# Performance work log

Hardware: AMD Instinct MI355X
Metric: run time of the kernel (lower is better)

## Reference

```python
import jax, jax.numpy as jnp
import numpy as np

B, S, H = 4, 2048, 1024

def setup_inputs() -> dict:
    key = jax.random.key(0)
    k = jax.random.split(key, 5)
    scale = 1.0 / np.sqrt(H)
    return {
        "hidden": jax.random.normal(k[0], (B, S, H), dtype=jnp.float32),
        "mask": jnp.zeros((B, 1, S, S), dtype=jnp.float32),
        "R": jax.random.normal(k[1], (S, S), dtype=jnp.float32),
        "G_w": jax.random.normal(k[2], (H, H), dtype=jnp.float32) * scale,
        "G_b": jnp.zeros((H,), dtype=jnp.float32),
        "F_w": jax.random.normal(k[3], (H, H), dtype=jnp.float32) * scale,
        "F_b": jnp.zeros((H,), dtype=jnp.float32),
    }

def reference(hidden, mask, R, G_w, G_b, F_w, F_b):
    # scores: [B, S, S] = learned random bias + additive attention mask
    scores = R + mask[:, 0]
    probs = jax.nn.softmax(scores, axis=-1)  # dropout is identity in eval mode
    values = jnp.einsum('bsh,oh->bso', hidden, G_w) + G_b  # G_linear
    out = jnp.einsum('bqk,bkh->bqh', probs, values)
    out = jnp.einsum('bsh,oh->bso', out, F_w) + F_b  # final_linear
    return out
```

## Files before the change

### kernel.cpp

```cpp
#include <hip/hip_runtime.h>
#include <hip/hip_bf16.h>

typedef __bf16 bf16x8 __attribute__((ext_vector_type(8)));
typedef __bf16 bf16x4 __attribute__((ext_vector_type(4)));
typedef float  f32x16 __attribute__((ext_vector_type(16)));

#define GPTR(p) ((__attribute__((address_space(1))) void*)(p))
#define LPTR(p) ((__attribute__((address_space(3))) void*)(p))

__global__ __launch_bounds__(256) void pre_kernel(
    const float* __restrict__ Fw, __bf16* __restrict__ f_bf,
    const float* __restrict__ Gw, __bf16* __restrict__ gt_bf,
    const float* __restrict__ Gb, const float* __restrict__ Fb,
    float* __restrict__ b2,
    const float* __restrict__ hidden, __bf16* __restrict__ xh, int H) {
    __shared__ float tile[64][65];
    const int blk = blockIdx.x;
    const int t = threadIdx.x;

    if (blk < 512) {
        long i = ((long)blk * 256 + t) * 8;
        float4 a = *reinterpret_cast<const float4*>(Fw + i);
        float4 c = *reinterpret_cast<const float4*>(Fw + i + 4);
        bf16x8 o;
        o[0] = (__bf16)a.x; o[1] = (__bf16)a.y; o[2] = (__bf16)a.z; o[3] = (__bf16)a.w;
        o[4] = (__bf16)c.x; o[5] = (__bf16)c.y; o[6] = (__bf16)c.z; o[7] = (__bf16)c.w;
        *reinterpret_cast<bf16x8*>(f_bf + i) = o;
    } else if (blk < 768) {
        const int id = blk - 512;
        const int bx = (id & 15) * 64;
        const int by = (id >> 4) * 64;
        const int tr = t >> 4;
        const int tc = (t & 15) * 4;
#pragma unroll
        for (int i = 0; i < 4; i++) {
            float4 v = *reinterpret_cast<const float4*>(&Gw[(size_t)(by + tr + i * 16) * H + bx + tc]);
            tile[tr + i * 16][tc + 0] = v.x;
            tile[tr + i * 16][tc + 1] = v.y;
            tile[tr + i * 16][tc + 2] = v.z;
            tile[tr + i * 16][tc + 3] = v.w;
        }
        __syncthreads();
        const int wr = t >> 2;
        const int wc = (t & 3) * 16;
        bf16x8 o0, o1;
#pragma unroll
        for (int j = 0; j < 8; j++) o0[j] = (__bf16)tile[wc + j][wr];
#pragma unroll
        for (int j = 0; j < 8; j++) o1[j] = (__bf16)tile[wc + 8 + j][wr];
        *reinterpret_cast<bf16x8*>(&gt_bf[(size_t)(bx + wr) * H + by + wc]) = o0;
        *reinterpret_cast<bf16x8*>(&gt_bf[(size_t)(bx + wr) * H + by + wc + 8]) = o1;
    } else if (blk < 1792) {
        const int o = blk - 768;
        float s = 0.f;
        for (int h = t; h < H; h += 256) s += Fw[(size_t)o * H + h] * Gb[h];
#pragma unroll
        for (int off = 32; off > 0; off >>= 1) s += __shfl_xor(s, off);
        __shared__ float ss[4];
        if ((t & 63) == 0) ss[t >> 6] = s;
        __syncthreads();
        if (t == 0) b2[o] = ss[0] + ss[1] + ss[2] + ss[3] + Fb[o];
    } else {
        const int id = blk - 1792;
        const long base = (long)id * 4096 + (long)t * 16;
        float4 v0 = *reinterpret_cast<const float4*>(hidden + base);
        float4 v1 = *reinterpret_cast<const float4*>(hidden + base + 4);
        float4 v2 = *reinterpret_cast<const float4*>(hidden + base + 8);
        float4 v3 = *reinterpret_cast<const float4*>(hidden + base + 12);
        bf16x8 o0, o1;
        o0[0] = (__bf16)v0.x; o0[1] = (__bf16)v0.y; o0[2] = (__bf16)v0.z; o0[3] = (__bf16)v0.w;
        o0[4] = (__bf16)v1.x; o0[5] = (__bf16)v1.y; o0[6] = (__bf16)v1.z; o0[7] = (__bf16)v1.w;
        o1[0] = (__bf16)v2.x; o1[1] = (__bf16)v2.y; o1[2] = (__bf16)v2.z; o1[3] = (__bf16)v2.w;
        o1[4] = (__bf16)v3.x; o1[5] = (__bf16)v3.y; o1[6] = (__bf16)v3.z; o1[7] = (__bf16)v3.w;
        *reinterpret_cast<bf16x8*>(xh + base) = o0;
        *reinterpret_cast<bf16x8*>(xh + base + 8) = o1;
    }
}

union MidSmem {
    struct { __bf16 a[64 * 64]; __bf16 b[64 * 64]; } g;
    float red[8];
};

__global__ __launch_bounds__(256) void mid_kernel(
    const __bf16* __restrict__ f_bf, const __bf16* __restrict__ gt_bf,
    __bf16* __restrict__ Wm,
    const float* __restrict__ R, const float* __restrict__ mask,
    __bf16* __restrict__ P, int H, int S) {
    __shared__ __align__(16) MidSmem sm;
    const int blk = blockIdx.x;
    const int t = threadIdx.x;

    if (blk < 256) {
        __bf16* As = sm.g.a;
        __bf16* Bs = sm.g.b;
        const int lane = t & 63;
        const int wave = t >> 6;
        const int lane31 = lane & 31;
        const int hi = lane >> 5;
        const int wm = (wave >> 1) * 32;
        const int wn = (wave & 1) * 32;
        const int bm = (blk >> 4) * 64;
        const int bn = (blk & 15) * 64;

        const int rsub = lane >> 3;
        const int csub = lane & 7;
        const int lchunk = csub ^ rsub;
        const __bf16* ga0 = f_bf + (size_t)(bm + wave * 16 + rsub) * H + lchunk * 8;
        const __bf16* gb0 = gt_bf + (size_t)(bn + wave * 16 + rsub) * H + lchunk * 8;

        f32x16 acc = (f32x16)(0.f);
        for (int kt = 0; kt < H; kt += 64) {
            __syncthreads();
#pragma unroll
            for (int c = 0; c < 2; c++)
                __builtin_amdgcn_global_load_lds(GPTR(ga0 + (size_t)(c * 8) * H + kt),
                                                 LPTR(&As[(wave * 16 + c * 8) * 64]), 16, 0, 0);
#pragma unroll
            for (int c = 0; c < 2; c++)
                __builtin_amdgcn_global_load_lds(GPTR(gb0 + (size_t)(c * 8) * H + kt),
                                                 LPTR(&Bs[(wave * 16 + c * 8) * 64]), 16, 0, 0);
            __syncthreads();
#pragma unroll
            for (int s = 0; s < 4; s++) {
                const int ra = wm + lane31;
                const int rb = wn + lane31;
                bf16x8 af = *reinterpret_cast<const bf16x8*>(
                    &As[ra * 64 + (((2 * s + hi) ^ (ra & 7)) << 3)]);
                bf16x8 bfr = *reinterpret_cast<const bf16x8*>(
                    &Bs[rb * 64 + (((2 * s + hi) ^ (rb & 7)) << 3)]);
                acc = __builtin_amdgcn_mfma_f32_32x32x16_bf16(af, bfr, acc, 0, 0, 0);
            }
        }
        const int cm = bm + wm;
        const int cn = bn + wn + lane31;
#pragma unroll
        for (int rq = 0; rq < 4; rq++) {
            const int rbase = rq * 8 + 4 * hi;
#pragma unroll
            for (int rr = 0; rr < 4; rr++)
                Wm[(size_t)(cm + rbase + rr) * H + cn] = (__bf16)acc[rq * 4 + rr];
        }
    } else {
        const int q = blk - 256;
        const int lane = t & 63, wave = t >> 6;
        const float* rrow = R + (size_t)q * S;

        float r[8];
#pragma unroll
        for (int i = 0; i < 2; i++) {
            float4 r4 = *reinterpret_cast<const float4*>(rrow + t * 8 + i * 4);
            r[i * 4 + 0] = r4.x; r[i * 4 + 1] = r4.y;
            r[i * 4 + 2] = r4.z; r[i * 4 + 3] = r4.w;
        }

        for (int b = 0; b < 4; b++) {
            const float* mrow = mask + ((size_t)b * S + q) * (size_t)S;
            __bf16* prow = P + ((size_t)b * S + q) * (size_t)S;

            float v[8];
#pragma unroll
            for (int i = 0; i < 2; i++) {
                float4 m4 = *reinterpret_cast<const float4*>(mrow + t * 8 + i * 4);
                v[i * 4 + 0] = r[i * 4 + 0] + m4.x;
                v[i * 4 + 1] = r[i * 4 + 1] + m4.y;
                v[i * 4 + 2] = r[i * 4 + 2] + m4.z;
                v[i * 4 + 3] = r[i * 4 + 3] + m4.w;
            }
            float mx = v[0];
#pragma unroll
            for (int i = 1; i < 8; i++) mx = fmaxf(mx, v[i]);
#pragma unroll
            for (int off = 32; off > 0; off >>= 1) mx = fmaxf(mx, __shfl_xor(mx, off));
            if (lane == 0) sm.red[wave] = mx;
            __syncthreads();
            mx = fmaxf(fmaxf(sm.red[0], sm.red[1]), fmaxf(sm.red[2], sm.red[3]));
            float sum = 0.f;
#pragma unroll
            for (int i = 0; i < 8; i++) { v[i] = __expf(v[i] - mx); sum += v[i]; }
#pragma unroll
            for (int off = 32; off > 0; off >>= 1) sum += __shfl_xor(sum, off);
            if (lane == 0) sm.red[4 + wave] = sum;
            __syncthreads();
            sum = sm.red[4] + sm.red[5] + sm.red[6] + sm.red[7];
            const float inv = 1.0f / sum;
            bf16x8 o;
#pragma unroll
            for (int i = 0; i < 8; i++) o[i] = (__bf16)(v[i] * inv);
            *reinterpret_cast<bf16x8*>(prow + t * 8) = o;
            __syncthreads();
        }
    }
}

__global__ __launch_bounds__(256) void gemm_wy_kernel(
    const __bf16* __restrict__ Wm, const __bf16* __restrict__ xh,
    __bf16* __restrict__ Yt) {
    constexpr int H = 1024, S = 2048, K = 1024;
    const int t = threadIdx.x;
    const int lane = t & 63;
    const int wave = t >> 6;
    const int lane31 = lane & 31;
    const int hi = lane >> 5;
    const int wm = (wave >> 1) * 64;
    const int wn = (wave & 1) * 64;
    const int id = blockIdx.x;
    const int xcd = id & 7;
    const int slot = id >> 3;
    const int bm = (slot & 7) * 128;
    const int bn = (xcd * 8 + (slot >> 3)) * 128;

    __shared__ __align__(16) __bf16 smem[32768];

    const int rsub = lane >> 3;
    const int csub = lane & 7;
    const int lchunk = csub ^ rsub;
    const __bf16* ga0 = Wm + (size_t)(bm + wave * 32 + rsub) * K + lchunk * 8;
    const __bf16* gb0 = xh + (size_t)(bn + wave * 32 + rsub) * K + lchunk * 8;

    auto stage = [&](int p, int kt) {
        __bf16* As_ = smem + p * 16384;
        __bf16* Bs_ = smem + p * 16384 + 8192;
#pragma unroll
        for (int c = 0; c < 4; c++)
            __builtin_amdgcn_global_load_lds(GPTR(ga0 + (size_t)(c * 8) * K + kt),
                                             LPTR(&As_[(wave * 32 + c * 8) * 64]), 16, 0, 0);
#pragma unroll
        for (int c = 0; c < 4; c++)
            __builtin_amdgcn_global_load_lds(GPTR(gb0 + (size_t)(c * 8) * K + kt),
                                             LPTR(&Bs_[(wave * 32 + c * 8) * 64]), 16, 0, 0);
    };

    f32x16 acc[2][2];
#pragma unroll
    for (int i = 0; i < 2; i++)
#pragma unroll
        for (int j = 0; j < 2; j++) acc[i][j] = (f32x16)(0.f);

    stage(0, 0);
    __syncthreads();
    int p = 0;
    for (int kt = 0; kt < K; kt += 64) {
        if (kt + 64 < K) stage(p ^ 1, kt + 64);
        const __bf16* As = smem + p * 16384;
        const __bf16* Bs = smem + p * 16384 + 8192;
#pragma unroll
        for (int s = 0; s < 4; s++) {
            bf16x8 af[2], bfr[2];
#pragma unroll
            for (int mi = 0; mi < 2; mi++) {
                const int r = wm + mi * 32 + lane31;
                af[mi] = *reinterpret_cast<const bf16x8*>(
                    &As[r * 64 + (((2 * s + hi) ^ (r & 7)) << 3)]);
            }
#pragma unroll
            for (int ni = 0; ni < 2; ni++) {
                const int r = wn + ni * 32 + lane31;
                bfr[ni] = *reinterpret_cast<const bf16x8*>(
                    &Bs[r * 64 + (((2 * s + hi) ^ (r & 7)) << 3)]);
            }
#pragma unroll
            for (int mi = 0; mi < 2; mi++)
#pragma unroll
                for (int ni = 0; ni < 2; ni++)
                    acc[mi][ni] = __builtin_amdgcn_mfma_f32_32x32x16_bf16(af[mi], bfr[ni], acc[mi][ni], 0, 0, 0);
        }
        __syncthreads();
        p ^= 1;
    }

#pragma unroll
    for (int mi = 0; mi < 2; mi++)
#pragma unroll
        for (int ni = 0; ni < 2; ni++) {
            const int cm = bm + wm + mi * 32;
            const int cnf = bn + wn + ni * 32 + lane31;
            __bf16* Cb = Yt + (size_t)(cnf >> 11) * H * S + (cnf & 2047);
#pragma unroll
            for (int rq = 0; rq < 4; rq++) {
                const int rbase = rq * 8 + 4 * hi;
#pragma unroll
                for (int rrq = 0; rrq < 4; rrq++)
                    Cb[(size_t)(cm + rbase + rrq) * S] = (__bf16)acc[mi][ni][rq * 4 + rrq];
            }
        }
}

template <bool CFLOAT, bool BIAS>
__global__ __launch_bounds__(256) void gemm_nt_kernel(
    const __bf16* __restrict__ A, const __bf16* __restrict__ B,
    const float* __restrict__ bias, void* __restrict__ Cv,
    int K, int lda, int ldb, int ldc,
    long strideA, long strideB, long strideC) {
    const int t = threadIdx.x;
    const int lane = t & 63;
    const int wave = t >> 6;
    const int lane31 = lane & 31;
    const int hi = lane >> 5;
    const int wm = (wave >> 1) * 64;
    const int wn = (wave & 1) * 64;
    const int id = blockIdx.x;
    const int xcd = id & 7;
    const int slot = id >> 3;
    const int bz = xcd >> 1;
    const int bm = ((xcd & 1) * 8 + (slot >> 3)) * 128;
    const int bn = (slot & 7) * 128;

    A += (size_t)bz * strideA;
    B += (size_t)bz * strideB;

    __shared__ __align__(16) __bf16 smem[32768];

    const int rsub = lane >> 3;
    const int csub = lane & 7;
    const int lchunk = csub ^ rsub;
    const __bf16* ga0 = A + (size_t)(bm + wave * 32 + rsub) * lda + lchunk * 8;
    const __bf16* gb0 = B + (size_t)(bn + wave * 32 + rsub) * ldb + lchunk * 8;

    auto stage = [&](int p, int kt) {
        __bf16* As_ = smem + p * 16384;
        __bf16* Bs_ = smem + p * 16384 + 8192;
#pragma unroll
        for (int c = 0; c < 4; c++)
            __builtin_amdgcn_global_load_lds(GPTR(ga0 + (size_t)(c * 8) * lda + kt),
                                             LPTR(&As_[(wave * 32 + c * 8) * 64]), 16, 0, 0);
#pragma unroll
        for (int c = 0; c < 4; c++)
            __builtin_amdgcn_global_load_lds(GPTR(gb0 + (size_t)(c * 8) * ldb + kt),
                                             LPTR(&Bs_[(wave * 32 + c * 8) * 64]), 16, 0, 0);
    };

    f32x16 acc[2][2];
#pragma unroll
    for (int i = 0; i < 2; i++)
#pragma unroll
        for (int j = 0; j < 2; j++) acc[i][j] = (f32x16)(0.f);

    stage(0, 0);
    __syncthreads();
    int p = 0;
    for (int kt = 0; kt < K; kt += 64) {
        if (kt + 64 < K) stage(p ^ 1, kt + 64);
        const __bf16* As = smem + p * 16384;
        const __bf16* Bs = smem + p * 16384 + 8192;
#pragma unroll
        for (int s = 0; s < 4; s++) {
            bf16x8 af[2], bfr[2];
#pragma unroll
            for (int mi = 0; mi < 2; mi++) {
                const int r = wm + mi * 32 + lane31;
                af[mi] = *reinterpret_cast<const bf16x8*>(
                    &As[r * 64 + (((2 * s + hi) ^ (r & 7)) << 3)]);
            }
#pragma unroll
            for (int ni = 0; ni < 2; ni++) {
                const int r = wn + ni * 32 + lane31;
                bfr[ni] = *reinterpret_cast<const bf16x8*>(
                    &Bs[r * 64 + (((2 * s + hi) ^ (r & 7)) << 3)]);
            }
#pragma unroll
            for (int mi = 0; mi < 2; mi++)
#pragma unroll
                for (int ni = 0; ni < 2; ni++)
                    acc[mi][ni] = __builtin_amdgcn_mfma_f32_32x32x16_bf16(af[mi], bfr[ni], acc[mi][ni], 0, 0, 0);
        }
        __syncthreads();
        p ^= 1;
    }

    __bf16* Cb = (__bf16*)Cv + (size_t)bz * strideC;
    float* Cf = (float*)Cv + (size_t)bz * strideC;
#pragma unroll
    for (int mi = 0; mi < 2; mi++)
#pragma unroll
        for (int ni = 0; ni < 2; ni++) {
            const int cm = bm + wm + mi * 32;
            const int cn = bn + wn + ni * 32 + lane31;
            const float bv = BIAS ? bias[cn] : 0.0f;
#pragma unroll
            for (int rq = 0; rq < 4; rq++) {
                const int rbase = rq * 8 + 4 * hi;
                if constexpr (CFLOAT) {
#pragma unroll
                    for (int rr = 0; rr < 4; rr++)
                        Cf[(size_t)(cm + rbase + rr) * ldc + cn] = acc[mi][ni][rq * 4 + rr] + bv;
                } else {
#pragma unroll
                    for (int rr = 0; rr < 4; rr++)
                        Cb[(size_t)(cm + rbase + rr) * ldc + cn] = (__bf16)(acc[mi][ni][rq * 4 + rr] + bv);
                }
            }
        }
}

extern "C" void kernel_launch(void* const* d_in, const int* in_sizes, int n_in,
                              void* d_out, int out_size, void* d_ws, size_t ws_size,
                              hipStream_t stream) {
    const float* hidden = (const float*)d_in[0];
    const float* mask   = (const float*)d_in[1];
    const float* R      = (const float*)d_in[2];
    const float* G_w    = (const float*)d_in[3];
    const float* G_b    = (const float*)d_in[4];
    const float* F_w    = (const float*)d_in[5];
    const float* F_b    = (const float*)d_in[6];
    float* out = (float*)d_out;

    constexpr int B = 4, S = 2048, H = 1024;
    char* ws = (char*)d_ws;
    __bf16* probs = (__bf16*)(ws);
    __bf16* yt    = (__bf16*)(ws + (32ll << 20));
    __bf16* xh    = (__bf16*)(ws + (48ll << 20));
    __bf16* f_bf  = (__bf16*)(ws + (64ll << 20));
    __bf16* gt_bf = (__bf16*)(ws + (66ll << 20));
    __bf16* Wm    = (__bf16*)(ws + (68ll << 20));
    float*  b2    = (float*)(ws + (70ll << 20));

    pre_kernel<<<3840, 256, 0, stream>>>(F_w, f_bf, G_w, gt_bf, G_b, F_b, b2,
                                         hidden, xh, H);

    mid_kernel<<<2304, 256, 0, stream>>>(f_bf, gt_bf, Wm, R, mask, probs, H, S);

    gemm_wy_kernel<<<512, 256, 0, stream>>>(Wm, xh, yt);

    gemm_nt_kernel<true, true><<<512, 256, 0, stream>>>(
        probs, yt, b2, out, S, S, S, H,
        (long)S * S, (long)H * S, (long)S * H);
}
```

Before: 228.4 us.

## Merge pre and mid kernels, convert weights to bf16 inside the W GEMM

Result: slower. 237.3 us (+3.9%).

```diff
diff --git a/kernel.cpp b/kernel.cpp
--- a/kernel.cpp
+++ b/kernel.cpp
@@ -8,60 +8,146 @@
 #define GPTR(p) ((__attribute__((address_space(1))) void*)(p))
 #define LPTR(p) ((__attribute__((address_space(3))) void*)(p))
 
-__global__ __launch_bounds__(256) void pre_kernel(
-    const float* __restrict__ Fw, __bf16* __restrict__ f_bf,
-    const float* __restrict__ Gw, __bf16* __restrict__ gt_bf,
+union MidSmem {
+    struct { __bf16 a[4096]; __bf16 b[4096]; float tile[32][65]; } g;
+    float red[8];
+};
+
+__global__ __launch_bounds__(256) void mid2_kernel(
+    const float* __restrict__ Fw, const float* __restrict__ Gw,
     const float* __restrict__ Gb, const float* __restrict__ Fb,
-    float* __restrict__ b2,
-    const float* __restrict__ hidden, __bf16* __restrict__ xh, int H) {
-    __shared__ float tile[64][65];
+    __bf16* __restrict__ Wm, float* __restrict__ b2,
+    const float* __restrict__ R, const float* __restrict__ mask,
+    __bf16* __restrict__ P,
+    const float* __restrict__ hidden, __bf16* __restrict__ xh,
+    int H, int S) {
+    __shared__ __align__(16) MidSmem sm;
     const int blk = blockIdx.x;
     const int t = threadIdx.x;
 
-    if (blk < 512) {
-        long i = ((long)blk * 256 + t) * 8;
-        float4 a = *reinterpret_cast<const float4*>(Fw + i);
-        float4 c = *reinterpret_cast<const float4*>(Fw + i + 4);
-        bf16x8 o;
-        o[0] = (__bf16)a.x; o[1] = (__bf16)a.y; o[2] = (__bf16)a.z; o[3] = (__bf16)a.w;
-        o[4] = (__bf16)c.x; o[5] = (__bf16)c.y; o[6] = (__bf16)c.z; o[7] = (__bf16)c.w;
-        *reinterpret_cast<bf16x8*>(f_bf + i) = o;
-    } else if (blk < 768) {
-        const int id = blk - 512;
-        const int bx = (id & 15) * 64;
-        const int by = (id >> 4) * 64;
-        const int tr = t >> 4;
-        const int tc = (t & 15) * 4;
-#pragma unroll
-        for (int i = 0; i < 4; i++) {
-            float4 v = *reinterpret_cast<const float4*>(&Gw[(size_t)(by + tr + i * 16) * H + bx + tc]);
-            tile[tr + i * 16][tc + 0] = v.x;
-            tile[tr + i * 16][tc + 1] = v.y;
-            tile[tr + i * 16][tc + 2] = v.z;
-            tile[tr + i * 16][tc + 3] = v.w;
-        }
-        __syncthreads();
-        const int wr = t >> 2;
-        const int wc = (t & 3) * 16;
-        bf16x8 o0, o1;
-#pragma unroll
-        for (int j = 0; j < 8; j++) o0[j] = (__bf16)tile[wc + j][wr];
-#pragma unroll
-        for (int j = 0; j < 8; j++) o1[j] = (__bf16)tile[wc + 8 + j][wr];
-        *reinterpret_cast<bf16x8*>(&gt_bf[(size_t)(bx + wr) * H + by + wc]) = o0;
-        *reinterpret_cast<bf16x8*>(&gt_bf[(size_t)(bx + wr) * H + by + wc + 8]) = o1;
-    } else if (blk < 1792) {
-        const int o = blk - 768;
-        float s = 0.f;
-        for (int h = t; h < H; h += 256) s += Fw[(size_t)o * H + h] * Gb[h];
-#pragma unroll
-        for (int off = 32; off > 0; off >>= 1) s += __shfl_xor(s, off);
-        __shared__ float ss[4];
-        if ((t & 63) == 0) ss[t >> 6] = s;
-        __syncthreads();
-        if (t == 0) b2[o] = ss[0] + ss[1] + ss[2] + ss[3] + Fb[o];
-    } else {
-        const int id = blk - 1792;
+    if (blk < 256) {
+        __bf16* As = sm.g.a;
+        __bf16* Bs = sm.g.b;
+        const int lane = t & 63;
+        const int wave = t >> 6;
+        const int lane31 = lane & 31;
+        const int hi = lane >> 5;
+        const int wm = (wave >> 1) * 32;
+        const int wn = (wave & 1) * 32;
+        const int bm = (blk >> 4) * 64;
+        const int bn = (blk & 15) * 64;
+
+        const int tr  = t >> 2;
+        const int tc2 = t & 3;
+        const int thh = t >> 3;
+        const int tkk = (t & 7) * 8;
+
+        f32x16 acc = (f32x16)(0.f);
+        for (int kt = 0; kt < H; kt += 64) {
+            __syncthreads();
+            {
+                const float* fr = Fw + (size_t)(bm + tr) * H + kt + tc2 * 16;
+                float4 fa0 = *reinterpret_cast<const float4*>(fr);
+                float4 fa1 = *reinterpret_cast<const float4*>(fr + 4);
+                float4 fa2 = *reinterpret_cast<const float4*>(fr + 8);
+                float4 fa3 = *reinterpret_cast<const float4*>(fr + 12);
+                bf16x8 w0, w1;
+                w0[0] = (__bf16)fa0.x; w0[1] = (__bf16)fa0.y; w0[2] = (__bf16)fa0.z; w0[3] = (__bf16)fa0.w;
+                w0[4] = (__bf16)fa1.x; w0[5] = (__bf16)fa1.y; w0[6] = (__bf16)fa1.z; w0[7] = (__bf16)fa1.w;
+                w1[0] = (__bf16)fa2.x; w1[1] = (__bf16)fa2.y; w1[2] = (__bf16)fa2.z; w1[3] = (__bf16)fa2.w;
+                w1[4] = (__bf16)fa3.x; w1[5] = (__bf16)fa3.y; w1[6] = (__bf16)fa3.z; w1[7] = (__bf16)fa3.w;
+                *reinterpret_cast<bf16x8*>(&As[tr * 64 + (((tc2 * 2) ^ (tr & 7)) << 3)]) = w0;
+                *reinterpret_cast<bf16x8*>(&As[tr * 64 + (((tc2 * 2 + 1) ^ (tr & 7)) << 3)]) = w1;
+            }
+#pragma unroll
+            for (int p = 0; p < 2; p++) {
+                const float* gr = Gw + (size_t)(kt + p * 32 + thh) * H + bn + tkk;
+                float4 g0 = *reinterpret_cast<const float4*>(gr);
+                float4 g1 = *reinterpret_cast<const float4*>(gr + 4);
+                sm.g.tile[thh][tkk + 0] = g0.x; sm.g.tile[thh][tkk + 1] = g0.y;
+                sm.g.tile[thh][tkk + 2] = g0.z; sm.g.tile[thh][tkk + 3] = g0.w;
+                sm.g.tile[thh][tkk + 4] = g1.x; sm.g.tile[thh][tkk + 5] = g1.y;
+                sm.g.tile[thh][tkk + 6] = g1.z; sm.g.tile[thh][tkk + 7] = g1.w;
+                __syncthreads();
+                const int cl = p * 4 + tc2;
+                bf16x8 ob;
+#pragma unroll
+                for (int e = 0; e < 8; e++)
+                    ob[e] = (__bf16)sm.g.tile[tc2 * 8 + e][tr];
+                *reinterpret_cast<bf16x8*>(&Bs[tr * 64 + ((cl ^ (tr & 7)) << 3)]) = ob;
+                __syncthreads();
+            }
+#pragma unroll
+            for (int s = 0; s < 4; s++) {
+                const int ra = wm + lane31;
+                const int rb = wn + lane31;
+                bf16x8 af = *reinterpret_cast<const bf16x8*>(
+                    &As[ra * 64 + (((2 * s + hi) ^ (ra & 7)) << 3)]);
+                bf16x8 bfr = *reinterpret_cast<const bf16x8*>(
+                    &Bs[rb * 64 + (((2 * s + hi) ^ (rb & 7)) << 3)]);
+                acc = __builtin_amdgcn_mfma_f32_32x32x16_bf16(af, bfr, acc, 0, 0, 0);
+            }
+        }
+        const int cm = bm + wm;
+        const int cn = bn + wn + lane31;
+#pragma unroll
+        for (int rq = 0; rq < 4; rq++) {
+            const int rbase = rq * 8 + 4 * hi;
+#pragma unroll
+            for (int rr = 0; rr < 4; rr++)
+                Wm[(size_t)(cm + rbase + rr) * H + cn] = (__bf16)acc[rq * 4 + rr];
+        }
+    } else if (blk < 2304) {
+        const int q = blk - 256;
+        const int lane = t & 63, wave = t >> 6;
+        const float* rrow = R + (size_t)q * S;
+
+        float r[8];
+#pragma unroll
+        for (int i = 0; i < 2; i++) {
+            float4 r4 = *reinterpret_cast<const float4*>(rrow + t * 8 + i * 4);
+            r[i * 4 + 0] = r4.x; r[i * 4 + 1] = r4.y;
+            r[i * 4 + 2] = r4.z; r[i * 4 + 3] = r4.w;
+        }
+
+        for (int b = 0; b < 4; b++) {
+            const float* mrow = mask + ((size_t)b * S + q) * (size_t)S;
+            __bf16* prow = P + ((size_t)b * S + q) * (size_t)S;
+
+            float v[8];
+#pragma unroll
+            for (int i = 0; i < 2; i++) {
+                float4 m4 = *reinterpret_cast<const float4*>(mrow + t * 8 + i * 4);
+                v[i * 4 + 0] = r[i * 4 + 0] + m4.x;
+                v[i * 4 + 1] = r[i * 4 + 1] + m4.y;
+                v[i * 4 + 2] = r[i * 4 + 2] + m4.z;
+                v[i * 4 + 3] = r[i * 4 + 3] + m4.w;
+            }
+            float mx = v[0];
+#pragma unroll
+            for (int i = 1; i < 8; i++) mx = fmaxf(mx, v[i]);
+#pragma unroll
+            for (int off = 32; off > 0; off >>= 1) mx = fmaxf(mx, __shfl_xor(mx, off));
+            if (lane == 0) sm.red[wave] = mx;
+            __syncthreads();
+            mx = fmaxf(fmaxf(sm.red[0], sm.red[1]), fmaxf(sm.red[2], sm.red[3]));
+            float sum = 0.f;
+#pragma unroll
+            for (int i = 0; i < 8; i++) { v[i] = __expf(v[i] - mx); sum += v[i]; }
+#pragma unroll
+            for (int off = 32; off > 0; off >>= 1) sum += __shfl_xor(sum, off);
+            if (lane == 0) sm.red[4 + wave] = sum;
+            __syncthreads();
+            sum = sm.red[4] + sm.red[5] + sm.red[6] + sm.red[7];
+            const float inv = 1.0f / sum;
+            bf16x8 o;
+#pragma unroll
+            for (int i = 0; i < 8; i++) o[i] = (__bf16)(v[i] * inv);
+            *reinterpret_cast<bf16x8*>(prow + t * 8) = o;
+            __syncthreads();
+        }
+    } else if (blk < 4352) {
+        const int id = blk - 2304;
         const long base = (long)id * 4096 + (long)t * 16;
         float4 v0 = *reinterpret_cast<const float4*>(hidden + base);
         float4 v1 = *reinterpret_cast<const float4*>(hidden + base + 4);
@@ -74,122 +160,15 @@
         o1[4] = (__bf16)v3.x; o1[5] = (__bf16)v3.y; o1[6] = (__bf16)v3.z; o1[7] = (__bf16)v3.w;
         *reinterpret_cast<bf16x8*>(xh + base) = o0;
         *reinterpret_cast<bf16x8*>(xh + base + 8) = o1;
-    }
-}
-
-union MidSmem {
-    struct { __bf16 a[64 * 64]; __bf16 b[64 * 64]; } g;
-    float red[8];
-};
-
-__global__ __launch_bounds__(256) void mid_kernel(
-    const __bf16* __restrict__ f_bf, const __bf16* __restrict__ gt_bf,
-    __bf16* __restrict__ Wm,
-    const float* __restrict__ R, const float* __restrict__ mask,
-    __bf16* __restrict__ P, int H, int S) {
-    __shared__ __align__(16) MidSmem sm;
-    const int blk = blockIdx.x;
-    const int t = threadIdx.x;
-
-    if (blk < 256) {
-        __bf16* As = sm.g.a;
-        __bf16* Bs = sm.g.b;
-        const int lane = t & 63;
-        const int wave = t >> 6;
-        const int lane31 = lane & 31;
-        const int hi = lane >> 5;
-        const int wm = (wave >> 1) * 32;
-        const int wn = (wave & 1) * 32;
-        const int bm = (blk >> 4) * 64;
-        const int bn = (blk & 15) * 64;
-
-        const int rsub = lane >> 3;
-        const int csub = lane & 7;
-        const int lchunk = csub ^ rsub;
-        const __bf16* ga0 = f_bf + (size_t)(bm + wave * 16 + rsub) * H + lchunk * 8;
-        const __bf16* gb0 = gt_bf + (size_t)(bn + wave * 16 + rsub) * H + lchunk * 8;
-
-        f32x16 acc = (f32x16)(0.f);
-        for (int kt = 0; kt < H; kt += 64) {
-            __syncthreads();
-#pragma unroll
-            for (int c = 0; c < 2; c++)
-                __builtin_amdgcn_global_load_lds(GPTR(ga0 + (size_t)(c * 8) * H + kt),
-                                                 LPTR(&As[(wave * 16 + c * 8) * 64]), 16, 0, 0);
-#pragma unroll
-            for (int c = 0; c < 2; c++)
-                __builtin_amdgcn_global_load_lds(GPTR(gb0 + (size_t)(c * 8) * H + kt),
-                                                 LPTR(&Bs[(wave * 16 + c * 8) * 64]), 16, 0, 0);
-            __syncthreads();
-#pragma unroll
-            for (int s = 0; s < 4; s++) {
-                const int ra = wm + lane31;
-                const int rb = wn + lane31;
-                bf16x8 af = *reinterpret_cast<const bf16x8*>(
-                    &As[ra * 64 + (((2 * s + hi) ^ (ra & 7)) << 3)]);
-                bf16x8 bfr = *reinterpret_cast<const bf16x8*>(
-                    &Bs[rb * 64 + (((2 * s + hi) ^ (rb & 7)) << 3)]);
-                acc = __builtin_amdgcn_mfma_f32_32x32x16_bf16(af, bfr, acc, 0, 0, 0);
-            }
-        }
-        const int cm = bm + wm;
-        const int cn = bn + wn + lane31;
-#pragma unroll
-        for (int rq = 0; rq < 4; rq++) {
-            const int rbase = rq * 8 + 4 * hi;
-#pragma unroll
-            for (int rr = 0; rr < 4; rr++)
-                Wm[(size_t)(cm + rbase + rr) * H + cn] = (__bf16)acc[rq * 4 + rr];
-        }
     } else {
-        const int q = blk - 256;
-        const int lane = t & 63, wave = t >> 6;
-        const float* rrow = R + (size_t)q * S;
-
-        float r[8];
-#pragma unroll
-        for (int i = 0; i < 2; i++) {
-            float4 r4 = *reinterpret_cast<const float4*>(rrow + t * 8 + i * 4);
-            r[i * 4 + 0] = r4.x; r[i * 4 + 1] = r4.y;
-            r[i * 4 + 2] = r4.z; r[i * 4 + 3] = r4.w;
-        }
-
-        for (int b = 0; b < 4; b++) {
-            const float* mrow = mask + ((size_t)b * S + q) * (size_t)S;
-            __bf16* prow = P + ((size_t)b * S + q) * (size_t)S;
-
-            float v[8];
-#pragma unroll
-            for (int i = 0; i < 2; i++) {
-                float4 m4 = *reinterpret_cast<const float4*>(mrow + t * 8 + i * 4);
-                v[i * 4 + 0] = r[i * 4 + 0] + m4.x;
-                v[i * 4 + 1] = r[i * 4 + 1] + m4.y;
-                v[i * 4 + 2] = r[i * 4 + 2] + m4.z;
-                v[i * 4 + 3] = r[i * 4 + 3] + m4.w;
-            }
-            float mx = v[0];
-#pragma unroll
-            for (int i = 1; i < 8; i++) mx = fmaxf(mx, v[i]);
-#pragma unroll
-            for (int off = 32; off > 0; off >>= 1) mx = fmaxf(mx, __shfl_xor(mx, off));
-            if (lane == 0) sm.red[wave] = mx;
-            __syncthreads();
-            mx = fmaxf(fmaxf(sm.red[0], sm.red[1]), fmaxf(sm.red[2], sm.red[3]));
-            float sum = 0.f;
-#pragma unroll
-            for (int i = 0; i < 8; i++) { v[i] = __expf(v[i] - mx); sum += v[i]; }
-#pragma unroll
-            for (int off = 32; off > 0; off >>= 1) sum += __shfl_xor(sum, off);
-            if (lane == 0) sm.red[4 + wave] = sum;
-            __syncthreads();
-            sum = sm.red[4] + sm.red[5] + sm.red[6] + sm.red[7];
-            const float inv = 1.0f / sum;
-            bf16x8 o;
-#pragma unroll
-            for (int i = 0; i < 8; i++) o[i] = (__bf16)(v[i] * inv);
-            *reinterpret_cast<bf16x8*>(prow + t * 8) = o;
-            __syncthreads();
-        }
+        const int o = blk - 4352;
+        float s = 0.f;
+        for (int h = t; h < H; h += 256) s += Fw[(size_t)o * H + h] * Gb[h];
+#pragma unroll
+        for (int off = 32; off > 0; off >>= 1) s += __shfl_xor(s, off);
+        if ((t & 63) == 0) sm.red[t >> 6] = s;
+        __syncthreads();
+        if (t == 0) b2[o] = sm.red[0] + sm.red[1] + sm.red[2] + sm.red[3] + Fb[o];
     }
 }
 
@@ -410,15 +389,11 @@
     __bf16* probs = (__bf16*)(ws);
     __bf16* yt    = (__bf16*)(ws + (32ll << 20));
     __bf16* xh    = (__bf16*)(ws + (48ll << 20));
-    __bf16* f_bf  = (__bf16*)(ws + (64ll << 20));
-    __bf16* gt_bf = (__bf16*)(ws + (66ll << 20));
-    __bf16* Wm    = (__bf16*)(ws + (68ll << 20));
-    float*  b2    = (float*)(ws + (70ll << 20));
-
-    pre_kernel<<<3840, 256, 0, stream>>>(F_w, f_bf, G_w, gt_bf, G_b, F_b, b2,
-                                         hidden, xh, H);
-
-    mid_kernel<<<2304, 256, 0, stream>>>(f_bf, gt_bf, Wm, R, mask, probs, H, S);
+    __bf16* Wm    = (__bf16*)(ws + (64ll << 20));
+    float*  b2    = (float*)(ws + (66ll << 20));
+
+    mid2_kernel<<<5376, 256, 0, stream>>>(F_w, G_w, G_b, F_b, Wm, b2,
+                                          R, mask, probs, hidden, xh, H, S);
 
     gemm_wy_kernel<<<512, 256, 0, stream>>>(Wm, xh, yt);
 
```
